# Optimization experiments

Hardware: AMD Instinct MI355X
Metric: run time of the kernel (lower is better)

## Reference

```python
import jax, jax.numpy as jnp
import numpy as np

GROUPSIZE = 128
ZERO_POINT = 8  # (maxq + 1) // 2 with maxq = 2**4 - 1


def setup_inputs() -> dict:
    key = jax.random.key(0)
    kA, ks, kq = jax.random.split(key, 3)
    M, K, N = 4096, 4096, 4096
    A = jax.random.normal(kA, (M, K), dtype=jnp.float32)
    # per-group scales, positive and small like real quantization scales
    s = jax.random.uniform(ks, (K // GROUPSIZE, N), dtype=jnp.float32) * 0.02 + 1e-3
    # int4 weights in [0, 15], packed 8 nibbles per int32 word along n
    nib = jax.random.randint(kq, (K, N), 0, 16, dtype=jnp.int32).astype(jnp.uint32)
    shifts = (4 * jnp.arange(8, dtype=jnp.uint32))
    q_u = (nib.reshape(K, N // 8, 8) << shifts).sum(axis=-1)  # uint32 (K, N//8)
    q = jax.lax.bitcast_convert_type(q_u, jnp.int32)
    return {"A": A, "s": s, "q": q}


def reference(A, s, q):
    # Unpack 8 int4 nibbles per int32 word: (K, N//8) -> (K, N)
    shifts = 4 * jnp.arange(8, dtype=jnp.int32)
    nib = (q[:, :, None] >> shifts) & 0xF  # (K, N//8, 8)
    nib = nib.reshape(q.shape[0], -1)      # (K, N)
    # Symmetric dequant with zero-point 8 and per-group (groupsize=128 rows) scales
    w = (nib.astype(A.dtype) - ZERO_POINT) * jnp.repeat(s.astype(A.dtype), GROUPSIZE, axis=0)
    return A @ w  # (M, N)
```

## Files before the change

kernel.cpp:

```cpp
#include <hip/hip_runtime.h>
#include <stdint.h>

#define GM 4096
#define GN 4096
#define GK 4096
#define QW (GN/8)

typedef __attribute__((ext_vector_type(4))) int   i32x4;
typedef __attribute__((ext_vector_type(8))) short bf16x8;
typedef __attribute__((ext_vector_type(4))) float f32x4;

#define AS1 __attribute__((address_space(1)))
#define AS3 __attribute__((address_space(3)))

static __device__ __forceinline__ void glds16(const void* g, void* l) {
  __builtin_amdgcn_global_load_lds((const AS1 uint32_t*)g, (AS3 uint32_t*)l, 16, 0, 0);
}

static __device__ __forceinline__ uint32_t bf16pack_rn(float hi, float lo) {
  uint32_t h = __float_as_uint(hi) + 0x8000u;
  uint32_t l = __float_as_uint(lo) + 0x8000u;
  return __builtin_amdgcn_perm(h, l, 0x07060302u);
}

static __device__ __forceinline__ uint32_t pack4i8(int b0, int b1, int b2, int b3) {
  return ((uint32_t)b0 & 255u) | (((uint32_t)b1 & 255u) << 8) |
         (((uint32_t)b2 & 255u) << 16) | (((uint32_t)b3 & 255u) << 24);
}

__global__ void __launch_bounds__(256) prep(const float* __restrict__ A,
                                            const float* __restrict__ S,
                                            const uint32_t* __restrict__ Q,
                                            int8_t* __restrict__ Ai,
                                            float* __restrict__ ascale,
                                            int8_t* __restrict__ Bf,
                                            float* __restrict__ wscale) {
  __shared__ uint32_t T32[128 * 32];
  __shared__ float4   red[8][32];
  __shared__ float    winv_l[128];

  const int b   = blockIdx.x;
  const int tid = threadIdx.x;

  if (b < 1024) {
    const int lane = tid & 63;
    const int row  = b * 4 + (tid >> 6);
    const float* src = A + (size_t)row * GK;
    float4 v[16];
    float m = 0.f;
    #pragma unroll
    for (int i = 0; i < 16; ++i) {
      v[i] = *(const float4*)(src + i * 256 + lane * 4);
      m = fmaxf(m, fmaxf(fmaxf(fabsf(v[i].x), fabsf(v[i].y)),
                         fmaxf(fabsf(v[i].z), fabsf(v[i].w))));
    }
    #pragma unroll
    for (int off = 32; off >= 1; off >>= 1)
      m = fmaxf(m, __shfl_xor(m, off, 64));
    const float rmax = fmaxf(m, 1e-20f);
    const float inv  = 127.0f / rmax;
    #pragma unroll
    for (int i = 0; i < 16; ++i) {
      uint32_t bb = pack4i8((int)__builtin_rintf(v[i].x * inv),
                            (int)__builtin_rintf(v[i].y * inv),
                            (int)__builtin_rintf(v[i].z * inv),
                            (int)__builtin_rintf(v[i].w * inv));
      *(uint32_t*)(Ai + (size_t)row * GK + i * 256 + lane * 4) = bb;
    }
    if (lane == 0) ascale[row] = rmax * (1.0f / 127.0f);
  } else if (b < 2048) {
    const int wb = b - 1024;
    const int n0 = (wb & 31) * 128;
    const int k0 = (wb >> 5) * 128;
    const int g  = wb >> 5;
    const int w  = tid & 15;
    const int kb = tid >> 4;

    {
      const int c4 = tid & 31;
      const int g8 = tid >> 5;
      float4 m4 = make_float4(0.f, 0.f, 0.f, 0.f);
      #pragma unroll
      for (int gg = 0; gg < 4; ++gg) {
        float4 sv = *(const float4*)(S + (size_t)(g8 * 4 + gg) * GN + n0 + c4 * 4);
        m4.x = fmaxf(m4.x, sv.x); m4.y = fmaxf(m4.y, sv.y);
        m4.z = fmaxf(m4.z, sv.z); m4.w = fmaxf(m4.w, sv.w);
      }
      red[g8][c4] = m4;
      __syncthreads();
      if (g8 == 0) {
        float4 m = red[0][c4];
        #pragma unroll
        for (int rr = 1; rr < 8; ++rr) {
          float4 o = red[rr][c4];
          m.x = fmaxf(m.x, o.x); m.y = fmaxf(m.y, o.y);
          m.z = fmaxf(m.z, o.z); m.w = fmaxf(m.w, o.w);
        }
        winv_l[c4 * 4 + 0] = 127.0f / (8.0f * m.x);
        winv_l[c4 * 4 + 1] = 127.0f / (8.0f * m.y);
        winv_l[c4 * 4 + 2] = 127.0f / (8.0f * m.z);
        winv_l[c4 * 4 + 3] = 127.0f / (8.0f * m.w);
      }
      __syncthreads();
    }

    float r[8], c[8];
    {
      const float* sp = S + (size_t)g * GN + n0 + w * 8;
      float4 sa = *(const float4*)sp, sb = *(const float4*)(sp + 4);
      float4 ia = *(const float4*)&winv_l[w * 8];
      float4 ib = *(const float4*)&winv_l[w * 8 + 4];
      const float sv[8] = {sa.x, sa.y, sa.z, sa.w, sb.x, sb.y, sb.z, sb.w};
      const float iv[8] = {ia.x, ia.y, ia.z, ia.w, ib.x, ib.y, ib.z, ib.w};
      #pragma unroll
      for (int j = 0; j < 8; ++j) { r[j] = sv[j] * iv[j]; c[j] = -8.0f * r[j]; }
    }

    const int swz = 4 * (w & 7);
    #pragma unroll
    for (int c2 = 0; c2 < 2; ++c2) {
      uint32_t q[4];
      #pragma unroll
      for (int i = 0; i < 4; ++i)
        q[i] = Q[(size_t)(k0 + c2 * 64 + kb * 4 + i) * QW + (n0 >> 3) + w];
      const int kword = c2 * 16 + kb;
      #pragma unroll
      for (int j = 0; j < 8; ++j) {
        int bb[4];
        #pragma unroll
        for (int i = 0; i < 4; ++i) {
          float nib = (float)((q[i] >> (4 * j)) & 0xFu);
          bb[i] = (int)__builtin_rintf(fmaf(nib, r[j], c[j]));
        }
        T32[(w * 8 + j) * 32 + (kword ^ swz)] = pack4i8(bb[0], bb[1], bb[2], bb[3]);
      }
    }
    __syncthreads();
    {
      const int l16 = tid & 63;
      const int sub = tid >> 6;
      #pragma unroll
      for (int p = 0; p < 4; ++p) {
        const int d     = p * 4 + sub;
        const int n16l  = d >> 1;
        const int kcl   = d & 1;
        const int col_l = n16l * 16 + (l16 & 15);
        const int gr    = (kcl << 2) | ((l16 >> 4) & 3);
        uint4 v = *(const uint4*)(&T32[col_l * 32 + ((gr ^ ((col_l >> 3) & 7)) << 2)]);
        const size_t n16g = (size_t)((n0 >> 4) + n16l);
        const size_t kcg  = (size_t)((k0 >> 6) + kcl);
        *(uint4*)(Bf + (((n16g << 6) + kcg) << 10) + (l16 << 4)) = v;
      }
    }
  } else {
    const int n = (b - 2048) * 256 + tid;
    float m = 0.f;
    #pragma unroll 8
    for (int gg = 0; gg < 32; ++gg) m = fmaxf(m, S[(size_t)gg * GN + n]);
    wscale[n] = m * (8.0f / 127.0f);
  }
}

__global__ void __launch_bounds__(512, 4) gemm_i8(const int8_t* __restrict__ Ai,
                                                  const int8_t* __restrict__ Bf,
                                                  const float* __restrict__ ascale,
                                                  const float* __restrict__ wscale,
                                                  float* __restrict__ C) {
  __shared__ __align__(16) int8_t As[4][64 * 128];

  const int tid = threadIdx.x;
  const int bid = blockIdx.y * gridDim.x + blockIdx.x;
  const int swb = ((bid & 7) << 6) | (bid >> 3);
  const int m0  = (swb >> 4) * 128;
  const int n0  = (swb & 15) * 256;

  const int lane = tid & 63;
  const int wid  = tid >> 6;
  const int wm   = wid >> 2;
  const int wn   = wid & 3;
  const int col  = lane & 15;
  const int quad = lane >> 4;

  const int sline = tid >> 3;
  const int sphys = tid & 7;
  const int sl    = sphys ^ (sline & 7);
  const int arow  = 2 * sline + (sl >> 2);
  const int kcs   = (sl & 3) << 4;
  const int8_t* Asrc = Ai + (size_t)(m0 + arow) * GK + kcs;

  const int n16b = (n0 >> 4) + wn * 4;
  const int8_t* Bp = Bf + ((size_t)n16b << 16) + (lane << 4);

  const int phq = (((col & 1) << 2) | quad) ^ (col >> 1);
  const int aRd = (wm * 32 + (col >> 1)) * 128 + phq * 16;

  i32x4 af[4], bfr[2][4];
  i32x4 acc[4][4];
  #pragma unroll
  for (int i = 0; i < 4; ++i)
    #pragma unroll
    for (int j = 0; j < 4; ++j)
      acc[i][j] = (i32x4){0, 0, 0, 0};

#define STAGE(b, ko) glds16(Asrc + (ko), &As[b][tid * 16])
#define LDBF(s, kc) do {                                                     \
    _Pragma("unroll")                                                        \
    for (int n_ = 0; n_ < 4; ++n_)                                           \
      bfr[s][n_] = *(const i32x4*)(Bp + ((size_t)n_ << 16)                   \
                                      + ((size_t)(kc) << 10));               \
  } while (0)
#define LDA_(b) do {                                                         \
    _Pragma("unroll")                                                        \
    for (int x_ = 0; x_ < 4; ++x_)                                           \
      af[x_] = *(const i32x4*)(&As[b][aRd + x_ * 1024]);                     \
  } while (0)
#define MFMA16_(s) do {                                                      \
    _Pragma("unroll")                                                        \
    for (int m_ = 0; m_ < 4; ++m_)                                           \
      _Pragma("unroll")                                                      \
      for (int n_ = 0; n_ < 4; ++n_)                                         \
        acc[m_][n_] = __builtin_amdgcn_mfma_i32_16x16x64_i8(                 \
            af[m_], bfr[s][n_], acc[m_][n_], 0, 0, 0);                       \
  } while (0)
#define VMW()   asm volatile("s_waitcnt vmcnt(1)" ::: "memory")
#define BARM()  asm volatile("s_barrier" ::: "memory")
#define PRIO1() __builtin_amdgcn_s_setprio(1)
#define PRIO0() __builtin_amdgcn_s_setprio(0)

#define STEP(T) do {                                                         \
    VMW();                           \
    BARM();                           \
    LDBF((T) + 1 < 64 ? ((T)+1) & 1 : 0, (T) + 1);         \
    STAGE(((T) + 2) & 3, (((T) + 2) & 63) << 6);          \
    LDA_((T) & 3);                                                           \
    PRIO1(); MFMA16_((T) & 1); PRIO0();                                      \
  } while (0)

  STAGE(0, 0);
  LDBF(0, 0);
  STAGE(1, 64);

  for (int it = 0; it < 16; ++it) {
    const int t = it * 4;
    STEP(t + 0);
    STEP(t + 1);
    STEP(t + 2);
    STEP(t + 3);
  }

  #pragma unroll
  for (int mt = 0; mt < 4; ++mt) {
    const int rbase = m0 + wm * 64 + mt * 16 + quad * 4;
    float4 a4 = *(const float4*)(ascale + rbase);
    const float ar[4] = {a4.x, a4.y, a4.z, a4.w};
    #pragma unroll
    for (int nt = 0; nt < 4; ++nt) {
      const int cbase = n0 + wn * 64 + nt * 16 + col;
      const float ws = wscale[cbase];
      #pragma unroll
      for (int r = 0; r < 4; ++r)
        C[(size_t)(rbase + r) * GN + cbase]
          = (float)acc[mt][nt][r] * (ar[r] * ws);
    }
  }
#undef STAGE
#undef LDBF
#undef LDA_
#undef MFMA16_
#undef VMW
#undef BARM
#undef PRIO1
#undef PRIO0
#undef STEP
}

#define BM 128
#define BN 128
#define BK 32

__global__ void __launch_bounds__(256) w4a32_gemm(
    const float* __restrict__ A,
    const float* __restrict__ S,
    const uint32_t* __restrict__ Q,
    float* __restrict__ C)
{
  __shared__ __align__(16) ushort As[BM*BK];
  __shared__ __align__(16) ushort Bs[BN*BK];

  const int tid  = threadIdx.x;
  const int m0   = blockIdx.y*BM;
  const int n0   = blockIdx.x*BN;
  const int wcol  = tid & 15;
  const int kpair = tid >> 4;
  const int ln   = tid & 63;
  const int wid  = tid >> 6;
  const int wm   = (wid >> 1) * 64;
  const int wn   = (wid & 1) * 64;
  const int col  = ln & 15;
  const int quad = ln >> 4;

  f32x4 acc[4][4];
  #pragma unroll
  for (int i=0;i<4;++i)
    #pragma unroll
    for (int j=0;j<4;++j)
      acc[i][j] = (f32x4){0.f,0.f,0.f,0.f};

  float sv[8], cv[8];
  float4 spf0, spf1;

  const float*    Abase = A + (size_t)m0 * GK;
  const uint32_t* Qbase = Q + (size_t)(n0>>3) + wcol;

  {
    const float* sp = S + n0 + wcol*8;
    spf0 = *(const float4*)sp;
    spf1 = *(const float4*)(sp + 4);
  }

  float4 a4[4];
  uint32_t wqa, wqb;
  #pragma unroll
  for (int i=0;i<4;++i) {
    int f = tid + i*256;
    a4[i] = *(const float4*)(Abase + (size_t)(f>>3)*GK + ((f&7)*4));
  }
  wqa = Qbase[(size_t)(2*kpair)   * QW];
  wqb = Qbase[(size_t)(2*kpair+1) * QW];

  for (int k0 = 0; k0 < GK; k0 += BK) {
    if ((k0 & 127) == 0) {
      sv[0]=spf0.x; sv[1]=spf0.y; sv[2]=spf0.z; sv[3]=spf0.w;
      sv[4]=spf1.x; sv[5]=spf1.y; sv[6]=spf1.z; sv[7]=spf1.w;
      #pragma unroll
      for (int j=0;j<8;++j) cv[j] = -8.0f * sv[j];
    }

    #pragma unroll
    for (int i=0;i<4;++i) {
      int f = tid + i*256;
      int row = f>>3, c4 = f&7;
      *(uint2*)(&As[row*BK + c4*4]) =
        make_uint2(bf16pack_rn(a4[i].y, a4[i].x), bf16pack_rn(a4[i].w, a4[i].z));
    }

    {
      const int kk = (2*kpair) ^ (8*(wcol&3));
      #pragma unroll
      for (int j=0;j<8;++j) {
        float fa = (float)((wqa >> (4*j)) & 0xFu);
        float fb = (float)((wqb >> (4*j)) & 0xFu);
        float wa = fmaf(fa, sv[j], cv[j]);
        float wb = fmaf(fb, sv[j], cv[j]);
        int n = wcol*8 + j;
        *(uint32_t*)(&Bs[n*BK + kk]) = bf16pack_rn(wb, wa);
      }
    }

    int kn = k0 + BK; if (kn >= GK) kn = 0;
    if ((kn & 127) == 0) {
      const float* sp = S + (size_t)(kn>>7)*GN + n0 + wcol*8;
      spf0 = *(const float4*)sp;
      spf1 = *(const float4*)(sp + 4);
    }
    #pragma unroll
    for (int i=0;i<4;++i) {
      int f = tid + i*256;
      a4[i] = *(const float4*)(Abase + (size_t)(f>>3)*GK + kn + ((f&7)*4));
    }
    wqa = Qbase[(size_t)(kn + 2*kpair)   * QW];
    wqb = Qbase[(size_t)(kn + 2*kpair+1) * QW];

    __syncthreads();

    bf16x8 af[4], bfr[4];
    #pragma unroll
    for (int t=0;t<4;++t) {
      af[t] = *(const bf16x8*)(&As[(wm + t*16 + col)*BK + quad*8]);
      int n = wn + t*16 + col;
      int kk = (quad*8) ^ (8*((n>>3)&3));
      bfr[t] = *(const bf16x8*)(&Bs[n*BK + kk]);
    }
    #pragma unroll
    for (int mt=0;mt<4;++mt)
      #pragma unroll
      for (int nt=0;nt<4;++nt)
        acc[mt][nt] = __builtin_amdgcn_mfma_f32_16x16x32_bf16(
                          af[mt], bfr[nt], acc[mt][nt], 0, 0, 0);

    __syncthreads();
  }

  #pragma unroll
  for (int mt=0;mt<4;++mt)
    #pragma unroll
    for (int nt=0;nt<4;++nt)
      #pragma unroll
      for (int r=0;r<4;++r)
        C[(size_t)(m0 + wm + mt*16 + quad*4 + r)*GN + n0 + wn + nt*16 + col]
          = acc[mt][nt][r];
}

extern "C" void kernel_launch(void* const* d_in, const int* in_sizes, int n_in,
                              void* d_out, int out_size, void* d_ws, size_t ws_size,
                              hipStream_t stream) {
  const float*    A = (const float*)d_in[0];
  const float*    S = (const float*)d_in[1];
  const uint32_t* Q = (const uint32_t*)d_in[2];
  float*          C = (float*)d_out;

  const size_t need = (size_t)GM * GK + (size_t)GN * GK + 3 * 4096 * 4 + 4096;
  if (ws_size >= need) {
    int8_t* Ai  = (int8_t*)d_ws;
    int8_t* Bfr = Ai + (size_t)GM * GK;
    float* ascale = (float*)(Bfr + (size_t)GN * GK);
    float* wscale = ascale + 4096;
    prep<<<dim3(1024 + 1024 + 16), dim3(256), 0, stream>>>(A, S, Q, Ai, ascale, Bfr, wscale);
    gemm_i8<<<dim3(16, 32), dim3(512), 0, stream>>>(Ai, Bfr, ascale, wscale, C);
  } else {
    w4a32_gemm<<<dim3(GN / BN, GM / BM), dim3(256), 0, stream>>>(A, S, Q, C);
  }
}
```

Baseline: 196.6 us.

## Load int8 A fragments directly from global, drop LDS staging and barriers

Rewrites the int8 GEMM so each wave reads its A fragments straight from global memory into registers, double-buffered alongside B, instead of staging A through a 4-deep LDS ring with barriers. Block tile shrinks from 128x256 with 512 threads to 128x128 with 256 threads, and blocks are assigned to XCDs so each XCD handles contiguous N columns. This removes barriers and LDS traffic, but A is no longer shared between waves through LDS, so global/L2 reads of A rise and the row-strided A loads are less coalesced.

```diff
diff --git a/kernel.cpp b/kernel.cpp
--- a/kernel.cpp
+++ b/kernel.cpp
@@ -161,40 +161,31 @@
   }
 }
 
-__global__ void __launch_bounds__(512, 4) gemm_i8(const int8_t* __restrict__ Ai,
-                                                  const int8_t* __restrict__ Bf,
-                                                  const float* __restrict__ ascale,
-                                                  const float* __restrict__ wscale,
-                                                  float* __restrict__ C) {
-  __shared__ __align__(16) int8_t As[4][64 * 128];
-
+__global__ void __launch_bounds__(256) gemm_i8(const int8_t* __restrict__ Ai,
+                                               const int8_t* __restrict__ Bf,
+                                               const float* __restrict__ ascale,
+                                               const float* __restrict__ wscale,
+                                               float* __restrict__ C) {
   const int tid = threadIdx.x;
-  const int bid = blockIdx.y * gridDim.x + blockIdx.x;
-  const int swb = ((bid & 7) << 6) | (bid >> 3);
-  const int m0  = (swb >> 4) * 128;
-  const int n0  = (swb & 15) * 256;
+  const int bid = blockIdx.x;
+  const int xcd = bid & 7;
+  const int s   = bid >> 3;
+  const int mi  = s >> 2;
+  const int ni  = (xcd << 2) | (s & 3);
+  const int m0  = mi * 128;
+  const int n0  = ni * 128;
 
   const int lane = tid & 63;
   const int wid  = tid >> 6;
-  const int wm   = wid >> 2;
-  const int wn   = wid & 3;
+  const int wm   = wid >> 1;
+  const int wn   = wid & 1;
   const int col  = lane & 15;
   const int quad = lane >> 4;
 
-  const int sline = tid >> 3;
-  const int sphys = tid & 7;
-  const int sl    = sphys ^ (sline & 7);
-  const int arow  = 2 * sline + (sl >> 2);
-  const int kcs   = (sl & 3) << 4;
-  const int8_t* Asrc = Ai + (size_t)(m0 + arow) * GK + kcs;
-
-  const int n16b = (n0 >> 4) + wn * 4;
-  const int8_t* Bp = Bf + ((size_t)n16b << 16) + (lane << 4);
-
-  const int phq = (((col & 1) << 2) | quad) ^ (col >> 1);
-  const int aRd = (wm * 32 + (col >> 1)) * 128 + phq * 16;
-
-  i32x4 af[4], bfr[2][4];
+  const int8_t* Ap = Ai + (size_t)(m0 + wm * 64 + col) * GK + quad * 16;
+  const int8_t* Bp = Bf + ((size_t)((n0 >> 4) + wn * 4) << 16) + (lane << 4);
+
+  i32x4 afr[2][4], bfr[2][4];
   i32x4 acc[4][4];
   #pragma unroll
   for (int i = 0; i < 4; ++i)
@@ -202,50 +193,37 @@
     for (int j = 0; j < 4; ++j)
       acc[i][j] = (i32x4){0, 0, 0, 0};
 
-#define STAGE(b, ko) glds16(Asrc + (ko), &As[b][tid * 16])
-#define LDBF(s, kc) do {                                                     \
+#define LDA(ss, kc) do {                                                     \
+    _Pragma("unroll")                                                        \
+    for (int m_ = 0; m_ < 4; ++m_)                                           \
+      afr[ss][m_] = *(const i32x4*)(Ap + (size_t)m_ * 16 * GK                \
+                                       + (size_t)(kc) * 64);                 \
+  } while (0)
+#define LDB(ss, kc) do {                                                     \
     _Pragma("unroll")                                                        \
     for (int n_ = 0; n_ < 4; ++n_)                                           \
-      bfr[s][n_] = *(const i32x4*)(Bp + ((size_t)n_ << 16)                   \
-                                      + ((size_t)(kc) << 10));               \
+      bfr[ss][n_] = *(const i32x4*)(Bp + ((size_t)n_ << 16)                  \
+                                       + ((size_t)(kc) << 10));              \
   } while (0)
-#define LDA_(b) do {                                                         \
-    _Pragma("unroll")                                                        \
-    for (int x_ = 0; x_ < 4; ++x_)                                           \
-      af[x_] = *(const i32x4*)(&As[b][aRd + x_ * 1024]);                     \
-  } while (0)
-#define MFMA16_(s) do {                                                      \
+#define MM(ss) do {                                                          \
     _Pragma("unroll")                                                        \
     for (int m_ = 0; m_ < 4; ++m_)                                           \
       _Pragma("unroll")                                                      \
       for (int n_ = 0; n_ < 4; ++n_)                                         \
         acc[m_][n_] = __builtin_amdgcn_mfma_i32_16x16x64_i8(                 \
-            af[m_], bfr[s][n_], acc[m_][n_], 0, 0, 0);                       \
+            afr[ss][m_], bfr[ss][n_], acc[m_][n_], 0, 0, 0);                 \
   } while (0)
-#define VMW()   asm volatile("s_waitcnt vmcnt(1)" ::: "memory")
-#define BARM()  asm volatile("s_barrier" ::: "memory")
-#define PRIO1() __builtin_amdgcn_s_setprio(1)
-#define PRIO0() __builtin_amdgcn_s_setprio(0)
-
-#define STEP(T) do {                                                         \
-    VMW();                           \
-    BARM();                           \
-    LDBF((T) + 1 < 64 ? ((T)+1) & 1 : 0, (T) + 1);         \
-    STAGE(((T) + 2) & 3, (((T) + 2) & 63) << 6);          \
-    LDA_((T) & 3);                                                           \
-    PRIO1(); MFMA16_((T) & 1); PRIO0();                                      \
-  } while (0)
-
-  STAGE(0, 0);
-  LDBF(0, 0);
-  STAGE(1, 64);
-
-  for (int it = 0; it < 16; ++it) {
-    const int t = it * 4;
-    STEP(t + 0);
-    STEP(t + 1);
-    STEP(t + 2);
-    STEP(t + 3);
+
+  LDA(0, 0); LDB(0, 0);
+  LDA(1, 1); LDB(1, 1);
+
+  for (int it = 0; it < 32; ++it) {
+    const int k2 = (2 * it + 2) & 63;
+    const int k3 = (2 * it + 3) & 63;
+    MM(0);
+    LDA(0, k2); LDB(0, k2);
+    MM(1);
+    LDA(1, k3); LDB(1, k3);
   }
 
   #pragma unroll
@@ -263,15 +241,9 @@
           = (float)acc[mt][nt][r] * (ar[r] * ws);
     }
   }
-#undef STAGE
-#undef LDBF
-#undef LDA_
-#undef MFMA16_
-#undef VMW
-#undef BARM
-#undef PRIO1
-#undef PRIO0
-#undef STEP
+#undef LDA
+#undef LDB
+#undef MM
 }
 
 #define BM 128
@@ -416,7 +388,7 @@
     float* ascale = (float*)(Bfr + (size_t)GN * GK);
     float* wscale = ascale + 4096;
     prep<<<dim3(1024 + 1024 + 16), dim3(256), 0, stream>>>(A, S, Q, Ai, ascale, Bfr, wscale);
-    gemm_i8<<<dim3(16, 32), dim3(512), 0, stream>>>(Ai, Bfr, ascale, wscale, C);
+    gemm_i8<<<dim3(1024), dim3(256), 0, stream>>>(Ai, Bfr, ascale, wscale, C);
   } else {
     w4a32_gemm<<<dim3(GN / BN, GM / BM), dim3(256), 0, stream>>>(A, S, Q, C);
   }
```

Result: slower. 270.6 us (+37.6%).
